# Kernel optimization log

Hardware: AMD Instinct MI355X
Metric: run time of the kernel (lower is better)

## Reference

```python
import jax, jax.numpy as jnp
import numpy as np

NUM_HEADS = 4
GN_GROUPS = 32
EPS = 1e-5


def setup_inputs() -> dict:
    key = jax.random.key(0)
    ks = jax.random.split(key, 6)
    B, C, H, W = 4, 256, 64, 64
    return {
        "x": jax.random.normal(ks[0], (B, C, H, W), dtype=jnp.float32),
        "gn_w": jnp.ones((C,), dtype=jnp.float32),
        "gn_b": jnp.zeros((C,), dtype=jnp.float32),
        "qkv_w": jax.random.normal(ks[1], (3 * C, C), dtype=jnp.float32) * 0.05,
        "qkv_b": jax.random.normal(ks[2], (3 * C,), dtype=jnp.float32) * 0.02,
        "proj_w": jax.random.normal(ks[3], (C, C), dtype=jnp.float32) * 0.05,
        "proj_b": jax.random.normal(ks[4], (C,), dtype=jnp.float32) * 0.02,
    }


def reference(x, gn_w, gn_b, qkv_w, qkv_b, proj_w, proj_b):
    b, c, h, w = x.shape
    L = h * w
    xf = x.reshape(b, c, L)

    # GroupNorm32: normalize over (channels_per_group, length) in float32
    xg = xf.reshape(b, GN_GROUPS, (c // GN_GROUPS) * L).astype(jnp.float32)
    mean = xg.mean(axis=-1, keepdims=True)
    var = xg.var(axis=-1, keepdims=True)
    xn = ((xg - mean) * jax.lax.rsqrt(var + EPS)).reshape(b, c, L).astype(x.dtype)
    xn = xn * gn_w[:, None] + gn_b[:, None]

    # 1x1 Conv1d == channel matmul: [3C, C] @ [b, C, L]
    qkv = jnp.einsum('oc,bcl->bol', qkv_w, xn) + qkv_b[:, None]

    # QKVAttentionLegacy
    ch = c // NUM_HEADS
    qkv_h = qkv.reshape(b * NUM_HEADS, 3 * ch, L)
    q, k, v = qkv_h[:, :ch], qkv_h[:, ch:2 * ch], qkv_h[:, 2 * ch:]
    scale = 1.0 / np.sqrt(np.sqrt(ch)).astype(np.float32)
    weight = jnp.einsum('bct,bcs->bts', q * scale, k * scale)  # [b*H, L, L]
    weight = jax.nn.softmax(weight.astype(jnp.float32), axis=-1).astype(qkv.dtype)
    a = jnp.einsum('bts,bcs->bct', weight, v).reshape(b, c, L)

    h_out = jnp.einsum('oc,bcl->bol', proj_w, a) + proj_b[:, None]
    return (xf + h_out).reshape(b, c, h, w)
```

## Files before the change

kernel.cpp:

```cpp
#include <hip/hip_runtime.h>
#include <math.h>

#define L 4096
#define C 256

typedef __attribute__((ext_vector_type(8))) short bf16x8;
typedef __attribute__((ext_vector_type(4))) short s16x4;
typedef __attribute__((ext_vector_type(4))) float f32x4;
typedef __attribute__((ext_vector_type(2))) unsigned int u32x2;
typedef __attribute__((ext_vector_type(4))) unsigned int u32x4;

#define MFMA16(a, b, c) __builtin_amdgcn_mfma_f32_16x16x32_bf16(a, b, c, 0, 0, 0)

static __device__ __forceinline__ short f2bf(float f) {
  union { float f; unsigned u; } x{f};
  unsigned r = (x.u + 0x7fffu + ((x.u >> 16) & 1u)) >> 16;
  return (short)r;
}
static __device__ __forceinline__ unsigned pack2(float a, float b) {
  return (unsigned)(unsigned short)f2bf(a) | ((unsigned)(unsigned short)f2bf(b) << 16);
}
static __device__ __forceinline__ unsigned ppack(float a, float b) {
  union { float f; unsigned u; } xa{a}, xb{b};
  return __builtin_amdgcn_perm(xb.u, xa.u, 0x07060302u);
}
static __device__ __forceinline__ void gload_lds16(const void* g, void* l) {
  __builtin_amdgcn_global_load_lds(
      (const __attribute__((address_space(1))) unsigned int*)g,
      (__attribute__((address_space(3))) unsigned int*)l, 16, 0, 0);
}

__global__ __launch_bounds__(256) void prep(const float* __restrict__ x,
    float* __restrict__ gnp, const float* __restrict__ wa,
    const float* __restrict__ wb, short* __restrict__ da,
    short* __restrict__ db) {
  int blk = blockIdx.x;
  int tid = threadIdx.x;
  if (blk < 512) {
    int bg = blk >> 2, q = blk & 3;
    const f32x4* xp = (const f32x4*)(x + (size_t)bg * 32768 + (size_t)q * 8192);
    float s = 0.f, ss = 0.f;
    #pragma unroll
    for (int i = 0; i < 8; ++i) {
      f32x4 v = xp[i * 256 + tid];
      s  += v[0] + v[1] + v[2] + v[3];
      ss += v[0]*v[0] + v[1]*v[1] + v[2]*v[2] + v[3]*v[3];
    }
    __shared__ float rs[256], rss[256];
    rs[tid] = s; rss[tid] = ss;
    __syncthreads();
    for (int off = 128; off > 0; off >>= 1) {
      if (tid < off) { rs[tid] += rs[tid + off]; rss[tid] += rss[tid + off]; }
      __syncthreads();
    }
    if (tid == 0) {
      gnp[(size_t)blk * 2]     = rs[0];
      gnp[(size_t)blk * 2 + 1] = rss[0];
    }
  } else {
    int i = (blk - 512) * 256 + tid;
    if (i < 768 * C) da[i] = f2bf(wa[i]);
    else db[i - 768 * C] = f2bf(wb[i - 768 * C]);
  }
}

__global__ __launch_bounds__(256) void gn_apply(const float* __restrict__ x,
    const float* __restrict__ gw, const float* __restrict__ gb,
    const float* __restrict__ gnp, short* __restrict__ xnT) {
  int bg = blockIdx.y;
  int b = bg >> 5, g = bg & 31;
  int tid = threadIdx.x;
  const float* xg = x + (size_t)bg * 32768;

  float s  = gnp[(size_t)(bg*4)*2]   + gnp[(size_t)(bg*4+1)*2] +
             gnp[(size_t)(bg*4+2)*2] + gnp[(size_t)(bg*4+3)*2];
  float ss = gnp[(size_t)(bg*4)*2+1]   + gnp[(size_t)(bg*4+1)*2+1] +
             gnp[(size_t)(bg*4+2)*2+1] + gnp[(size_t)(bg*4+3)*2+1];
  float mean = s * (1.f / 32768.f);
  float var  = ss * (1.f / 32768.f) - mean * mean;
  float rstd = rsqrtf(var + 1e-5f);

  float scl[8], sft[8];
  #pragma unroll
  for (int c = 0; c < 8; ++c) {
    float wv = gw[g * 8 + c], bv = gb[g * 8 + c];
    scl[c] = rstd * wv;
    sft[c] = bv - mean * rstd * wv;
  }

  short* outb = xnT + (size_t)b * L * C + g * 8;
  int lb = blockIdx.x * 1024 + tid * 4;
  f32x4 v[8];
  #pragma unroll
  for (int c = 0; c < 8; ++c)
    v[c] = *(const f32x4*)(xg + (size_t)c * L + lb);
  #pragma unroll
  for (int j = 0; j < 4; ++j) {
    u32x4 ov;
    #pragma unroll
    for (int cp = 0; cp < 4; ++cp)
      ov[cp] = pack2(v[2*cp][j]   * scl[2*cp]   + sft[2*cp],
                     v[2*cp+1][j] * scl[2*cp+1] + sft[2*cp+1]);
    *(u32x4*)(outb + (size_t)(lb + j) * C) = ov;
  }
}

__global__ __launch_bounds__(256) void qkv_mfma(const short* __restrict__ wq,
    const float* __restrict__ bias, const short* __restrict__ xnT,
    short* __restrict__ qT, short* __restrict__ kT, short* __restrict__ vB) {
  int tid = threadIdx.x;
  int wid = tid >> 6, lane = tid & 63, g = lane >> 4, lr = lane & 15;
  int oy = blockIdx.y;
  int o0 = oy * 64;
  int b  = blockIdx.z;
  int head = oy / 3, kind = oy % 3;
  int bh = b * 4 + head;
  int lw = blockIdx.x * 128 + wid * 32;
  const short* xb = xnT + (size_t)b * L * C;

  f32x4 acc[4][2];
  #pragma unroll
  for (int m = 0; m < 4; ++m)
    #pragma unroll
    for (int nt = 0; nt < 2; ++nt) acc[m][nt] = (f32x4)0.f;

  #pragma unroll 2
  for (int k0 = 0; k0 < C; k0 += 32) {
    bf16x8 af[4], bfr[2];
    #pragma unroll
    for (int m = 0; m < 4; ++m)
      af[m] = *(const bf16x8*)(wq + (size_t)(o0 + m * 16 + lr) * C + k0 + g * 8);
    #pragma unroll
    for (int nt = 0; nt < 2; ++nt)
      bfr[nt] = *(const bf16x8*)(xb + (size_t)(lw + nt * 16 + lr) * C + k0 + g * 8);
    #pragma unroll
    for (int m = 0; m < 4; ++m)
      #pragma unroll
      for (int nt = 0; nt < 2; ++nt)
        acc[m][nt] = MFMA16(af[m], bfr[nt], acc[m][nt]);
  }

  float sc = (kind == 0) ? 0.51014930f : (kind == 1) ? 0.35355339f : 1.0f;
  if (kind == 2) {
    #pragma unroll
    for (int m = 0; m < 4; ++m)
      #pragma unroll
      for (int nt = 0; nt < 2; ++nt)
        #pragma unroll
        for (int r = 0; r < 4; ++r) {
          int o = m * 16 + g * 4 + r;
          vB[((size_t)bh * 64 + o) * L + lw + nt * 16 + lr] =
              f2bf(acc[m][nt][r] + bias[o0 + o]);
        }
  } else {
    short* dst = (kind == 0 ? qT : kT);
    #pragma unroll
    for (int m = 0; m < 4; ++m)
      #pragma unroll
      for (int nt = 0; nt < 2; ++nt) {
        s16x4 pk;
        #pragma unroll
        for (int r = 0; r < 4; ++r)
          pk[r] = f2bf((acc[m][nt][r] + bias[o0 + m * 16 + g * 4 + r]) * sc);
        *(s16x4*)(dst + ((size_t)bh * L + lw + nt * 16 + lr) * 64 + m * 16 + g * 4) = pk;
      }
  }
}

__global__ __launch_bounds__(512) void attn_mfma(
    const short* __restrict__ qT, const short* __restrict__ kT,
    const short* __restrict__ vB, short* __restrict__ amatT) {
  int orig = blockIdx.x;
  int bid = (orig & 7) * 32 + (orig >> 3);
  int bh = bid >> 4, qb = bid & 15;
  int b = bh >> 2, h = bh & 3;
  int tid = threadIdx.x;
  int wid = tid >> 6, lane = tid & 63;
  int g = lane >> 4, lr = lane & 15;
  int tw = qb * 256 + wid * 32;
  int lx7 = lr & 7;
  int pswA = ((lr & 3) << 4) | ((lr >> 2) << 2);

  const short* qTh = qT + (size_t)bh * L * 64;
  const short* kTh = kT + (size_t)bh * L * 64;
  const short* vh  = vB + (size_t)bh * 64 * L;

  __shared__ short Kt[4][64 * 64];
  __shared__ short Vt[4][64 * 64];
  __shared__ short plds[8][32][64];

  bf16x8 qf[2][2];
  #pragma unroll
  for (int nt = 0; nt < 2; ++nt)
    #pragma unroll
    for (int ks = 0; ks < 2; ++ks)
      qf[nt][ks] = *(const bf16x8*)(qTh + (size_t)(tw + nt * 16 + lr) * 64 +
                                    ks * 32 + g * 8);

  bf16x8 ones;
  #pragma unroll
  for (int i = 0; i < 8; ++i) ones[i] = (short)0x3F80;

  f32x4 acc[4][2], acc_l[2];
  #pragma unroll
  for (int cm = 0; cm < 4; ++cm)
    #pragma unroll
    for (int nt = 0; nt < 2; ++nt) acc[cm][nt] = (f32x4)0.f;
  acc_l[0] = (f32x4)0.f; acc_l[1] = (f32x4)0.f;

  size_t koff, voff;
  int ldsc;
  {
    int r = tid >> 3, c16 = tid & 7;
    int cs = c16 ^ (r & 7);
    koff = (size_t)r * 64 + cs * 8;
    voff = (size_t)r * L + cs * 8;
    ldsc = wid * 512;
  }

  gload_lds16(kTh + koff, &Kt[0][ldsc]);
  gload_lds16(vh + voff, &Vt[0][ldsc]);
  gload_lds16(kTh + koff + (size_t)64 * 64, &Kt[1][ldsc]);
  gload_lds16(vh + voff + 64, &Vt[1][ldsc]);

  int sl = 0;
  #pragma unroll 1
  for (int s = 0; s < 32; ++s) {
    if (s < 31) {
      int nb = sl ^ 2;
      size_t t0 = (size_t)(2 * s + 2) * 64, t1 = (size_t)(2 * s + 3) * 64;
      gload_lds16(kTh + koff + t0 * 64, &Kt[nb][ldsc]);
      gload_lds16(vh + voff + t0, &Vt[nb][ldsc]);
      gload_lds16(kTh + koff + t1 * 64, &Kt[nb + 1][ldsc]);
      gload_lds16(vh + voff + t1, &Vt[nb + 1][ldsc]);
      asm volatile("s_waitcnt vmcnt(4)" ::: "memory");
    } else {
      asm volatile("s_waitcnt vmcnt(0)" ::: "memory");
    }
    __builtin_amdgcn_sched_barrier(0);
    __builtin_amdgcn_s_barrier();

    const short* Ka = &Kt[sl][0];     const short* Va = &Vt[sl][0];
    const short* Kb = &Kt[sl + 1][0]; const short* Vb = &Vt[sl + 1][0];

    f32x4 st0[4][2], st1[4][2];
    __builtin_amdgcn_s_setprio(1);
    #pragma unroll
    for (int sm = 0; sm < 4; ++sm) {
      int row = sm * 16 + lr;
      bf16x8 kf0 = *(const bf16x8*)&Ka[row * 64 + (g ^ lx7) * 8];
      bf16x8 kf1 = *(const bf16x8*)&Ka[row * 64 + ((4 + g) ^ lx7) * 8];
      #pragma unroll
      for (int nt = 0; nt < 2; ++nt) {
        f32x4 cc = (f32x4)0.f;
        cc = MFMA16(kf0, qf[nt][0], cc);
        cc = MFMA16(kf1, qf[nt][1], cc);
        st0[sm][nt] = cc;
      }
    }
    __builtin_amdgcn_s_setprio(0);
    #pragma unroll
    for (int sm = 0; sm < 4; ++sm) {
      int row = sm * 16 + lr;
      bf16x8 kf0 = *(const bf16x8*)&Kb[row * 64 + (g ^ lx7) * 8];
      bf16x8 kf1 = *(const bf16x8*)&Kb[row * 64 + ((4 + g) ^ lx7) * 8];
      #pragma unroll
      for (int nt = 0; nt < 2; ++nt) {
        f32x4 cc = (f32x4)0.f;
        cc = MFMA16(kf0, qf[nt][0], cc);
        cc = MFMA16(kf1, qf[nt][1], cc);
        st1[sm][nt] = cc;
        u32x2 w;
        w[0] = ppack(__builtin_amdgcn_exp2f(st0[sm][nt][0]),
                     __builtin_amdgcn_exp2f(st0[sm][nt][1]));
        w[1] = ppack(__builtin_amdgcn_exp2f(st0[sm][nt][2]),
                     __builtin_amdgcn_exp2f(st0[sm][nt][3]));
        *(u32x2*)&plds[wid][nt * 16 + lr][(sm * 16 + g * 4) ^ pswA] = w;
      }
    }
    bf16x8 pf0[2][2];
    #pragma unroll
    for (int nt = 0; nt < 2; ++nt)
      #pragma unroll
      for (int ks = 0; ks < 2; ++ks) {
        s16x4 pa = *(const s16x4*)&plds[wid][nt * 16 + lr][(ks * 32 + g * 8) ^ pswA];
        s16x4 pb = *(const s16x4*)&plds[wid][nt * 16 + lr][(ks * 32 + g * 8 + 4) ^ pswA];
        pf0[nt][ks] = __builtin_shufflevector(pa, pb, 0, 1, 2, 3, 4, 5, 6, 7);
      }
    #pragma unroll
    for (int nt = 0; nt < 2; ++nt) {
      acc_l[nt] = MFMA16(ones, pf0[nt][0], acc_l[nt]);
      acc_l[nt] = MFMA16(ones, pf0[nt][1], acc_l[nt]);
    }
    #pragma unroll
    for (int cm = 0; cm < 4; ++cm) {
      int row = cm * 16 + lr;
      bf16x8 vf0 = *(const bf16x8*)&Va[row * 64 + (g ^ lx7) * 8];
      bf16x8 vf1 = *(const bf16x8*)&Va[row * 64 + ((4 + g) ^ lx7) * 8];
      #pragma unroll
      for (int nt = 0; nt < 2; ++nt) {
        acc[cm][nt] = MFMA16(vf0, pf0[nt][0], acc[cm][nt]);
        acc[cm][nt] = MFMA16(vf1, pf0[nt][1], acc[cm][nt]);
        u32x2 w;
        w[0] = ppack(__builtin_amdgcn_exp2f(st1[cm][nt][0]),
                     __builtin_amdgcn_exp2f(st1[cm][nt][1]));
        w[1] = ppack(__builtin_amdgcn_exp2f(st1[cm][nt][2]),
                     __builtin_amdgcn_exp2f(st1[cm][nt][3]));
        *(u32x2*)&plds[wid][nt * 16 + lr][(cm * 16 + g * 4) ^ pswA] = w;
      }
    }
    bf16x8 pf1[2][2];
    #pragma unroll
    for (int nt = 0; nt < 2; ++nt)
      #pragma unroll
      for (int ks = 0; ks < 2; ++ks) {
        s16x4 pa = *(const s16x4*)&plds[wid][nt * 16 + lr][(ks * 32 + g * 8) ^ pswA];
        s16x4 pb = *(const s16x4*)&plds[wid][nt * 16 + lr][(ks * 32 + g * 8 + 4) ^ pswA];
        pf1[nt][ks] = __builtin_shufflevector(pa, pb, 0, 1, 2, 3, 4, 5, 6, 7);
      }
    __builtin_amdgcn_s_setprio(1);
    #pragma unroll
    for (int nt = 0; nt < 2; ++nt) {
      acc_l[nt] = MFMA16(ones, pf1[nt][0], acc_l[nt]);
      acc_l[nt] = MFMA16(ones, pf1[nt][1], acc_l[nt]);
    }
    #pragma unroll
    for (int cm = 0; cm < 4; ++cm) {
      int row = cm * 16 + lr;
      bf16x8 vf0 = *(const bf16x8*)&Vb[row * 64 + (g ^ lx7) * 8];
      bf16x8 vf1 = *(const bf16x8*)&Vb[row * 64 + ((4 + g) ^ lx7) * 8];
      #pragma unroll
      for (int nt = 0; nt < 2; ++nt) {
        acc[cm][nt] = MFMA16(vf0, pf1[nt][0], acc[cm][nt]);
        acc[cm][nt] = MFMA16(vf1, pf1[nt][1], acc[cm][nt]);
      }
    }
    __builtin_amdgcn_s_setprio(0);
    __builtin_amdgcn_s_barrier();
    sl ^= 2;
  }

  #pragma unroll
  for (int nt = 0; nt < 2; ++nt) {
    float inv = 1.f / acc_l[nt][0];
    #pragma unroll
    for (int cm = 0; cm < 4; ++cm) {
      s16x4 pk;
      #pragma unroll
      for (int r = 0; r < 4; ++r) pk[r] = f2bf(acc[cm][nt][r] * inv);
      *(s16x4*)(amatT + ((size_t)b * L + tw + nt * 16 + lr) * C + h * 64 +
                cm * 16 + g * 4) = pk;
    }
  }
}

__global__ __launch_bounds__(256) void proj_mfma(const short* __restrict__ pw,
    const float* __restrict__ bias, const short* __restrict__ amatT,
    const float* __restrict__ xres, float* __restrict__ out) {
  int tid = threadIdx.x;
  int wid = tid >> 6, lane = tid & 63, g = lane >> 4, lr = lane & 15;
  int o0 = blockIdx.y * 64;
  int b  = blockIdx.z;
  int lw = blockIdx.x * 128 + wid * 32;
  const short* ab = amatT + (size_t)b * L * C;

  f32x4 acc[4][2];
  #pragma unroll
  for (int m = 0; m < 4; ++m)
    #pragma unroll
    for (int nt = 0; nt < 2; ++nt) acc[m][nt] = (f32x4)0.f;

  #pragma unroll 2
  for (int k0 = 0; k0 < C; k0 += 32) {
    bf16x8 af[4], bfr[2];
    #pragma unroll
    for (int m = 0; m < 4; ++m)
      af[m] = *(const bf16x8*)(pw + (size_t)(o0 + m * 16 + lr) * C + k0 + g * 8);
    #pragma unroll
    for (int nt = 0; nt < 2; ++nt)
      bfr[nt] = *(const bf16x8*)(ab + (size_t)(lw + nt * 16 + lr) * C + k0 + g * 8);
    #pragma unroll
    for (int m = 0; m < 4; ++m)
      #pragma unroll
      for (int nt = 0; nt < 2; ++nt)
        acc[m][nt] = MFMA16(af[m], bfr[nt], acc[m][nt]);
  }

  #pragma unroll
  for (int m = 0; m < 4; ++m)
    #pragma unroll
    for (int nt = 0; nt < 2; ++nt)
      #pragma unroll
      for (int r = 0; r < 4; ++r) {
        int o = o0 + m * 16 + g * 4 + r;
        size_t idx = ((size_t)b * C + o) * L + lw + nt * 16 + lr;
        out[idx] = acc[m][nt][r] + bias[o] + xres[idx];
      }
}

extern "C" void kernel_launch(void* const* d_in, const int* in_sizes, int n_in,
                              void* d_out, int out_size, void* d_ws, size_t ws_size,
                              hipStream_t stream) {
  const float* x      = (const float*)d_in[0];
  const float* gn_w   = (const float*)d_in[1];
  const float* gn_b   = (const float*)d_in[2];
  const float* qkv_w  = (const float*)d_in[3];
  const float* qkv_b  = (const float*)d_in[4];
  const float* proj_w = (const float*)d_in[5];
  const float* proj_b = (const float*)d_in[6];
  float* out = (float*)d_out;

  short* xnT   = (short*)d_ws;
  short* qT    = xnT   + (size_t)4 * L * C;
  short* kT    = qT    + (size_t)16 * L * 64;
  short* vB    = kT    + (size_t)16 * L * 64;
  short* amatT = vB    + (size_t)16 * L * 64;
  short* wqbf  = amatT + (size_t)4 * L * C;
  short* pwbf  = wqbf  + (size_t)768 * C;
  float* gnp   = (float*)(pwbf + (size_t)C * C);

  prep<<<1536, 256, 0, stream>>>(x, gnp, qkv_w, proj_w, wqbf, pwbf);
  gn_apply<<<dim3(4, 128), 256, 0, stream>>>(x, gn_w, gn_b, gnp, xnT);
  qkv_mfma<<<dim3(32, 12, 4), 256, 0, stream>>>(wqbf, qkv_b, xnT, qT, kT, vB);
  attn_mfma<<<256, 512, 0, stream>>>(qT, kT, vB, amatT);
  proj_mfma<<<dim3(32, 4, 4), 256, 0, stream>>>(pwbf, proj_b, amatT, x, out);
}
```

Measured before the change: 148.9 us.

## Process one KV tile per iteration with a three-buffer rotating LDS ring

The attention loop now handles one 64-key tile per iteration instead of two, over 64 iterations. It prefetches two tiles ahead into a three-slot K/V shared-memory ring instead of the four-slot double-pair scheme. This drops the manual interleave of the second tile's QK MFMAs with the first tile's exp/pack, which reduces live registers (one score array) and cuts K/V LDS from four slots to three. That may allow more resident blocks per CU. The cost is twice as many barrier pairs and less instruction-level overlap between exp and MFMA work.

```diff
diff --git a/kernel.cpp b/kernel.cpp
--- a/kernel.cpp
+++ b/kernel.cpp
@@ -185,8 +185,8 @@
   const short* kTh = kT + (size_t)bh * L * 64;
   const short* vh  = vB + (size_t)bh * 64 * L;
 
-  __shared__ short Kt[4][64 * 64];
-  __shared__ short Vt[4][64 * 64];
+  __shared__ short Kt[3][64 * 64];
+  __shared__ short Vt[3][64 * 64];
   __shared__ short plds[8][32][64];
 
   bf16x8 qf[2][2];
@@ -218,126 +218,92 @@
     ldsc = wid * 512;
   }
 
-  gload_lds16(kTh + koff, &Kt[0][ldsc]);
-  gload_lds16(vh + voff, &Vt[0][ldsc]);
-  gload_lds16(kTh + koff + (size_t)64 * 64, &Kt[1][ldsc]);
-  gload_lds16(vh + voff + 64, &Vt[1][ldsc]);
-
-  int sl = 0;
+  #define STAGE(buf, s0v)                                              \
+    {                                                                  \
+      gload_lds16(kTh + koff + (size_t)(s0v) * 64, &Kt[buf][ldsc]);    \
+      gload_lds16(vh + voff + (size_t)(s0v), &Vt[buf][ldsc]);          \
+    }
+
+  STAGE(0, 0);
+  STAGE(1, 64);
+
+  int cur = 0;
   #pragma unroll 1
-  for (int s = 0; s < 32; ++s) {
-    if (s < 31) {
-      int nb = sl ^ 2;
-      size_t t0 = (size_t)(2 * s + 2) * 64, t1 = (size_t)(2 * s + 3) * 64;
-      gload_lds16(kTh + koff + t0 * 64, &Kt[nb][ldsc]);
-      gload_lds16(vh + voff + t0, &Vt[nb][ldsc]);
-      gload_lds16(kTh + koff + t1 * 64, &Kt[nb + 1][ldsc]);
-      gload_lds16(vh + voff + t1, &Vt[nb + 1][ldsc]);
+  for (int t = 0; t < 64; ++t) {
+    if (t < 62) {
+      int nb = (cur == 2) ? 0 : cur + 1;
+      nb = (nb == 2) ? 0 : nb + 1;
+      STAGE(nb, (t + 2) * 64);
       asm volatile("s_waitcnt vmcnt(4)" ::: "memory");
+    } else if (t == 62) {
+      asm volatile("s_waitcnt vmcnt(2)" ::: "memory");
     } else {
       asm volatile("s_waitcnt vmcnt(0)" ::: "memory");
     }
     __builtin_amdgcn_sched_barrier(0);
     __builtin_amdgcn_s_barrier();
 
-    const short* Ka = &Kt[sl][0];     const short* Va = &Vt[sl][0];
-    const short* Kb = &Kt[sl + 1][0]; const short* Vb = &Vt[sl + 1][0];
-
-    f32x4 st0[4][2], st1[4][2];
+    const short* Ka = &Kt[cur][0];
+    const short* Va = &Vt[cur][0];
+
+    f32x4 st[4][2];
     __builtin_amdgcn_s_setprio(1);
     #pragma unroll
     for (int sm = 0; sm < 4; ++sm) {
       int row = sm * 16 + lr;
-      bf16x8 kf0 = *(const bf16x8*)&Ka[row * 64 + (g ^ lx7) * 8];
-      bf16x8 kf1 = *(const bf16x8*)&Ka[row * 64 + ((4 + g) ^ lx7) * 8];
+      bf16x8 kf0 = *(const bf16x8*)&Ka[row * 64 + ((g ^ lx7)) * 8];
+      bf16x8 kf1 = *(const bf16x8*)&Ka[row * 64 + (((4 + g) ^ lx7)) * 8];
       #pragma unroll
       for (int nt = 0; nt < 2; ++nt) {
         f32x4 cc = (f32x4)0.f;
         cc = MFMA16(kf0, qf[nt][0], cc);
         cc = MFMA16(kf1, qf[nt][1], cc);
-        st0[sm][nt] = cc;
+        st[sm][nt] = cc;
       }
     }
     __builtin_amdgcn_s_setprio(0);
-    #pragma unroll
-    for (int sm = 0; sm < 4; ++sm) {
-      int row = sm * 16 + lr;
-      bf16x8 kf0 = *(const bf16x8*)&Kb[row * 64 + (g ^ lx7) * 8];
-      bf16x8 kf1 = *(const bf16x8*)&Kb[row * 64 + ((4 + g) ^ lx7) * 8];
+
+    #pragma unroll
+    for (int sm = 0; sm < 4; ++sm)
       #pragma unroll
       for (int nt = 0; nt < 2; ++nt) {
-        f32x4 cc = (f32x4)0.f;
-        cc = MFMA16(kf0, qf[nt][0], cc);
-        cc = MFMA16(kf1, qf[nt][1], cc);
-        st1[sm][nt] = cc;
         u32x2 w;
-        w[0] = ppack(__builtin_amdgcn_exp2f(st0[sm][nt][0]),
-                     __builtin_amdgcn_exp2f(st0[sm][nt][1]));
-        w[1] = ppack(__builtin_amdgcn_exp2f(st0[sm][nt][2]),
-                     __builtin_amdgcn_exp2f(st0[sm][nt][3]));
+        w[0] = ppack(__builtin_amdgcn_exp2f(st[sm][nt][0]),
+                     __builtin_amdgcn_exp2f(st[sm][nt][1]));
+        w[1] = ppack(__builtin_amdgcn_exp2f(st[sm][nt][2]),
+                     __builtin_amdgcn_exp2f(st[sm][nt][3]));
         *(u32x2*)&plds[wid][nt * 16 + lr][(sm * 16 + g * 4) ^ pswA] = w;
       }
-    }
-    bf16x8 pf0[2][2];
+
+    bf16x8 pf[2][2];
     #pragma unroll
     for (int nt = 0; nt < 2; ++nt)
       #pragma unroll
       for (int ks = 0; ks < 2; ++ks) {
         s16x4 pa = *(const s16x4*)&plds[wid][nt * 16 + lr][(ks * 32 + g * 8) ^ pswA];
         s16x4 pb = *(const s16x4*)&plds[wid][nt * 16 + lr][(ks * 32 + g * 8 + 4) ^ pswA];
-        pf0[nt][ks] = __builtin_shufflevector(pa, pb, 0, 1, 2, 3, 4, 5, 6, 7);
-      }
+        pf[nt][ks] = __builtin_shufflevector(pa, pb, 0, 1, 2, 3, 4, 5, 6, 7);
+      }
+    __builtin_amdgcn_s_setprio(1);
     #pragma unroll
     for (int nt = 0; nt < 2; ++nt) {
-      acc_l[nt] = MFMA16(ones, pf0[nt][0], acc_l[nt]);
-      acc_l[nt] = MFMA16(ones, pf0[nt][1], acc_l[nt]);
+      acc_l[nt] = MFMA16(ones, pf[nt][0], acc_l[nt]);
+      acc_l[nt] = MFMA16(ones, pf[nt][1], acc_l[nt]);
     }
     #pragma unroll
     for (int cm = 0; cm < 4; ++cm) {
       int row = cm * 16 + lr;
-      bf16x8 vf0 = *(const bf16x8*)&Va[row * 64 + (g ^ lx7) * 8];
-      bf16x8 vf1 = *(const bf16x8*)&Va[row * 64 + ((4 + g) ^ lx7) * 8];
+      bf16x8 vf0 = *(const bf16x8*)&Va[row * 64 + ((g ^ lx7)) * 8];
+      bf16x8 vf1 = *(const bf16x8*)&Va[row * 64 + (((4 + g) ^ lx7)) * 8];
       #pragma unroll
       for (int nt = 0; nt < 2; ++nt) {
-        acc[cm][nt] = MFMA16(vf0, pf0[nt][0], acc[cm][nt]);
-        acc[cm][nt] = MFMA16(vf1, pf0[nt][1], acc[cm][nt]);
-        u32x2 w;
-        w[0] = ppack(__builtin_amdgcn_exp2f(st1[cm][nt][0]),
-                     __builtin_amdgcn_exp2f(st1[cm][nt][1]));
-        w[1] = ppack(__builtin_amdgcn_exp2f(st1[cm][nt][2]),
-                     __builtin_amdgcn_exp2f(st1[cm][nt][3]));
-        *(u32x2*)&plds[wid][nt * 16 + lr][(cm * 16 + g * 4) ^ pswA] = w;
-      }
-    }
-    bf16x8 pf1[2][2];
-    #pragma unroll
-    for (int nt = 0; nt < 2; ++nt)
-      #pragma unroll
-      for (int ks = 0; ks < 2; ++ks) {
-        s16x4 pa = *(const s16x4*)&plds[wid][nt * 16 + lr][(ks * 32 + g * 8) ^ pswA];
-        s16x4 pb = *(const s16x4*)&plds[wid][nt * 16 + lr][(ks * 32 + g * 8 + 4) ^ pswA];
-        pf1[nt][ks] = __builtin_shufflevector(pa, pb, 0, 1, 2, 3, 4, 5, 6, 7);
-      }
-    __builtin_amdgcn_s_setprio(1);
-    #pragma unroll
-    for (int nt = 0; nt < 2; ++nt) {
-      acc_l[nt] = MFMA16(ones, pf1[nt][0], acc_l[nt]);
-      acc_l[nt] = MFMA16(ones, pf1[nt][1], acc_l[nt]);
-    }
-    #pragma unroll
-    for (int cm = 0; cm < 4; ++cm) {
-      int row = cm * 16 + lr;
-      bf16x8 vf0 = *(const bf16x8*)&Vb[row * 64 + (g ^ lx7) * 8];
-      bf16x8 vf1 = *(const bf16x8*)&Vb[row * 64 + ((4 + g) ^ lx7) * 8];
-      #pragma unroll
-      for (int nt = 0; nt < 2; ++nt) {
-        acc[cm][nt] = MFMA16(vf0, pf1[nt][0], acc[cm][nt]);
-        acc[cm][nt] = MFMA16(vf1, pf1[nt][1], acc[cm][nt]);
+        acc[cm][nt] = MFMA16(vf0, pf[nt][0], acc[cm][nt]);
+        acc[cm][nt] = MFMA16(vf1, pf[nt][1], acc[cm][nt]);
       }
     }
     __builtin_amdgcn_s_setprio(0);
     __builtin_amdgcn_s_barrier();
-    sl ^= 2;
+    cur = (cur == 2) ? 0 : cur + 1;
   }
 
   #pragma unroll
@@ -352,6 +318,7 @@
                 cm * 16 + g * 4) = pk;
     }
   }
+  #undef STAGE
 }
 
 __global__ __launch_bounds__(256) void proj_mfma(const short* __restrict__ pw,
```

After: 163.6 us. 9.9% more time.
